# Optimization experiments

Hardware: AMD Instinct MI355X
Metric: run time of the kernel (lower is better)

The kernel has to match this reference:

```python
import jax, jax.numpy as jnp
import numpy as np

INPUT_SIZE = 4
HIDDEN_SIZE = 4
SEQ_LEN = 2048
BATCH = 4096


def _lstm_layer(x, W_ih, W_hh, b_ih, b_hh):
    """Single-layer LSTM over x: [T, B, I]; PyTorch gate order (i, f, g, o)."""
    H = W_hh.shape[1]
    B = x.shape[1]
    # Precompute the input projection for all timesteps (one big GEMM).
    xg = jnp.einsum('tbi,gi->tbg', x, W_ih) + (b_ih + b_hh)  # [T, B, 4H]

    def step(carry, xg_t):
        h, c = carry
        gates = xg_t + h @ W_hh.T  # [B, 4H]
        i, f, g, o = jnp.split(gates, 4, axis=-1)
        i = jax.nn.sigmoid(i)
        f = jax.nn.sigmoid(f)
        g = jnp.tanh(g)
        o = jax.nn.sigmoid(o)
        c = f * c + i * g
        h = o * jnp.tanh(c)
        return (h, c), h

    h0 = jnp.zeros((B, H), x.dtype)
    c0 = jnp.zeros((B, H), x.dtype)
    _, ys = jax.lax.scan(step, (h0, c0), xg)
    return ys  # [T, B, H]


def setup_inputs() -> dict:
    key = jax.random.key(0)
    ks = jax.random.split(key, 9)
    bound = 1.0 / np.sqrt(HIDDEN_SIZE)  # torch LSTM init: U(-1/sqrt(H), 1/sqrt(H))

    def u(k, shape):
        return jax.random.uniform(k, shape, jnp.float32, -bound, bound)

    x = jax.random.normal(ks[0], (SEQ_LEN, BATCH, INPUT_SIZE), jnp.float32)
    return {
        'x': x,
        'W_ih0': u(ks[1], (4 * HIDDEN_SIZE, INPUT_SIZE)),
        'W_hh0': u(ks[2], (4 * HIDDEN_SIZE, HIDDEN_SIZE)),
        'b_ih0': u(ks[3], (4 * HIDDEN_SIZE,)),
        'b_hh0': u(ks[4], (4 * HIDDEN_SIZE,)),
        'W_ih1': u(ks[5], (4 * HIDDEN_SIZE, HIDDEN_SIZE)),
        'W_hh1': u(ks[6], (4 * HIDDEN_SIZE, HIDDEN_SIZE)),
        'b_ih1': u(ks[7], (4 * HIDDEN_SIZE,)),
        'b_hh1': u(ks[8], (4 * HIDDEN_SIZE,)),
    }


def reference(x, W_ih0, W_hh0, b_ih0, b_hh0, W_ih1, W_hh1, b_ih1, b_hh1):
    h1 = _lstm_layer(x, W_ih0, W_hh0, b_ih0, b_hh0)
    h2 = _lstm_layer(h1, W_ih1, W_hh1, b_ih1, b_hh1)
    return h2  # [T, B, H], matching `x, _ = self.lstm(x); return x`
```

## Files before the change

kernel.cpp:

```cpp
#include <hip/hip_runtime.h>

#define SEQ_T   2048
#define BATCH_N 4096
#define LOG2E   1.4426950408889634f
#define K_SEG   16
#define NSEG    (SEQ_T / K_SEG)

#define DPPF(v, ctrl) __int_as_float(__builtin_amdgcn_mov_dpp(__float_as_int(v), (ctrl), 0xF, 0xF, true))
#define RHM 0x141
#define MIR 0x140

__global__ __launch_bounds__(128, 2) void lstm2_split(
    const float* __restrict__ x,
    const float* __restrict__ Wih0, const float* __restrict__ Whh0,
    const float* __restrict__ bih0, const float* __restrict__ bhh0,
    const float* __restrict__ Wih1, const float* __restrict__ Whh1,
    const float* __restrict__ bih1, const float* __restrict__ bhh1,
    float* __restrict__ out)
{
    __shared__ float ring[32][4][4];

    const int wv    = threadIdx.x >> 6;
    const int lane  = threadIdx.x & 63;
    const int cpos  = lane >> 4;
    const int g16   = lane & 15;
    const int u     = g16 >> 2;
    const int r     = g16 & 3;
    const int row   = r * 4 + u;
    const int chain = blockIdx.x * 4 + cpos;
    const bool isA  = (wv == 0);

    const float srow = (r == 2) ? (-2.0f * LOG2E) : (-LOG2E);
    float win[4], whh[4], bb;
    if (isA) {
#pragma unroll
        for (int d = 0; d < 4; ++d) {
            win[d] = Wih0[row * 4 + d]       * srow;
            whh[d] = Whh0[row * 4 + (u ^ d)] * srow;
        }
        bb = (bih0[row] + bhh0[row]) * srow;
    } else {
#pragma unroll
        for (int d = 0; d < 4; ++d) {
            win[d] = Wih1[row * 4 + d]       * srow;
            whh[d] = Whh1[row * 4 + (u ^ d)] * srow;
        }
        bb = (bih1[row] + bhh1[row]) * srow;
    }
    const float csc = -2.0f * LOG2E;
    const float ka = (r == 2) ? 2.0f * csc : 1.0f;
    const float kb = (r == 2) ? -csc       : 0.0f;

    const char* __restrict__ xb = (const char*)x;
    char* __restrict__ ob = (char*)out;

    float h = 0.f, ha = 0.f, hb2 = 0.f, hc = 0.f;
    float cs = 0.f;

    auto cell = [&](float acc) {
        acc = fmaf(whh[0], h, fmaf(whh[1], ha,
              fmaf(whh[2], hb2, fmaf(whh[3], hc, acc))));
        float e = __builtin_amdgcn_exp2f(acc);
        float s = __builtin_amdgcn_rcpf(1.0f + e);
        float a = fmaf(ka, s, kb);
        float iv = DPPF(a, 0x00), fv = DPPF(a, 0x55);
        float gv = DPPF(a, 0xAA), ov = DPPF(a, 0xFF);
        cs = fmaf(fv, cs, iv * gv);
        float z  = __builtin_amdgcn_exp2f(cs);
        float t2 = fmaf(2.0f, __builtin_amdgcn_rcpf(1.0f + z), -1.0f);
        h  = ov * t2;
        ha = DPPF(h, RHM);
        hc = DPPF(h, MIR);
        hb2 = DPPF(ha, MIR);
    };

    if (isA) {
        const unsigned xhome = (unsigned)chain * 16u;
        const unsigned XCL   = xhome + 2047u * 65536u;
        float4 xbuf[8];
        unsigned xoff = xhome;
#pragma unroll
        for (int i = 0; i < 8; ++i) {
            xbuf[i] = *(const float4*)(xb + xoff);
            xoff += 65536u;
        }
        for (int seg = 0; seg <= NSEG; ++seg) {
            __syncthreads();
            if (seg < NSEG) {
                float (*slot)[4] = ring[(seg & 1) * K_SEG];
#pragma unroll
                for (int i = 0; i < K_SEG; ++i) {
                    const float4 xv = xbuf[i & 7];
                    unsigned off = (xoff < XCL) ? xoff : XCL;
                    xbuf[i & 7] = *(const float4*)(xb + off);
                    xoff += 65536u;
                    float acc = fmaf(win[0], xv.x, fmaf(win[1], xv.y,
                                fmaf(win[2], xv.z, fmaf(win[3], xv.w, bb))));
                    cell(acc);
                    if (r == 0) slot[i * 4 + cpos][u] = h;
                }
            }
        }
    } else {
        unsigned ooff = (unsigned)(chain * 16 + u * 4);
        for (int seg = 0; seg <= NSEG; ++seg) {
            __syncthreads();
            if (seg > 0) {
                const float (*slot)[4] = ring[((seg - 1) & 1) * K_SEG];
                float4 hr[8];
#pragma unroll
                for (int hf = 0; hf < 2; ++hf) {
#pragma unroll
                    for (int s = 0; s < 8; ++s)
                        hr[s] = *(const float4*)&slot[(hf * 8 + s) * 4 + cpos][0];
#pragma unroll
                    for (int i = 0; i < 8; ++i) {
                        const float4 X = hr[i];
                        float acc = fmaf(win[0], X.x, fmaf(win[1], X.y,
                                    fmaf(win[2], X.z, fmaf(win[3], X.w, bb))));
                        cell(acc);
                        if (r == 0) *(float*)(ob + ooff) = h;
                        ooff += 65536u;
                    }
                }
            }
        }
    }
}

extern "C" void kernel_launch(void* const* d_in, const int* in_sizes, int n_in,
                              void* d_out, int out_size, void* d_ws, size_t ws_size,
                              hipStream_t stream) {
    const float* x    = (const float*)d_in[0];
    const float* Wih0 = (const float*)d_in[1];
    const float* Whh0 = (const float*)d_in[2];
    const float* bih0 = (const float*)d_in[3];
    const float* bhh0 = (const float*)d_in[4];
    const float* Wih1 = (const float*)d_in[5];
    const float* Whh1 = (const float*)d_in[6];
    const float* bih1 = (const float*)d_in[7];
    const float* bhh1 = (const float*)d_in[8];
    float* out = (float*)d_out;

    dim3 grid(1024), block(128);
    hipLaunchKernelGGL(lstm2_split, grid, block, 0, stream,
                       x, Wih0, Whh0, bih0, bhh0, Wih1, Whh1, bih1, bhh1, out);
}
```

Baseline: 258.8 us.

## Move layer-1 input projection into layer-0 wave and pass preactivations via LDS

The layer-0 wave now also computes the layer-1 input projection (W_ih1·h + bias) right after each step and writes one preactivation per gate row into a widened LDS ring. The layer-1 wave then only reads a scalar per step and runs the recurrent cell, which takes four FMAs off its serial critical path. The last segment is peeled so the x-load address clamp only runs there. In exchange the layer-0 wave does more work per step, every lane now writes to LDS, and the shared ring is four times larger.

```diff
diff --git a/kernel.cpp b/kernel.cpp
--- a/kernel.cpp
+++ b/kernel.cpp
@@ -18,7 +18,7 @@
     const float* __restrict__ bih1, const float* __restrict__ bhh1,
     float* __restrict__ out)
 {
-    __shared__ float ring[32][4][4];
+    __shared__ float ring[32][4][16];
 
     const int wv    = threadIdx.x >> 6;
     const int lane  = threadIdx.x & 63;
@@ -31,31 +31,12 @@
     const bool isA  = (wv == 0);
 
     const float srow = (r == 2) ? (-2.0f * LOG2E) : (-LOG2E);
-    float win[4], whh[4], bb;
-    if (isA) {
-#pragma unroll
-        for (int d = 0; d < 4; ++d) {
-            win[d] = Wih0[row * 4 + d]       * srow;
-            whh[d] = Whh0[row * 4 + (u ^ d)] * srow;
-        }
-        bb = (bih0[row] + bhh0[row]) * srow;
-    } else {
-#pragma unroll
-        for (int d = 0; d < 4; ++d) {
-            win[d] = Wih1[row * 4 + d]       * srow;
-            whh[d] = Whh1[row * 4 + (u ^ d)] * srow;
-        }
-        bb = (bih1[row] + bhh1[row]) * srow;
-    }
     const float csc = -2.0f * LOG2E;
     const float ka = (r == 2) ? 2.0f * csc : 1.0f;
     const float kb = (r == 2) ? -csc       : 0.0f;
 
-    const char* __restrict__ xb = (const char*)x;
-    char* __restrict__ ob = (char*)out;
-
-    float h = 0.f, ha = 0.f, hb2 = 0.f, hc = 0.f;
-    float cs = 0.f;
+    float whh[4];
+    float h = 0.f, ha = 0.f, hb2 = 0.f, hc = 0.f, cs = 0.f;
 
     auto cell = [&](float acc) {
         acc = fmaf(whh[0], h, fmaf(whh[1], ha,
@@ -74,7 +55,20 @@
         hb2 = DPPF(ha, MIR);
     };
 
+    const char* __restrict__ xb = (const char*)x;
+    char* __restrict__ ob = (char*)out;
+
     if (isA) {
+        float win[4], wpx[4];
+#pragma unroll
+        for (int d = 0; d < 4; ++d) {
+            win[d] = Wih0[row * 4 + d]       * srow;
+            whh[d] = Whh0[row * 4 + (u ^ d)] * srow;
+            wpx[d] = Wih1[row * 4 + (u ^ d)] * srow;
+        }
+        const float bb  = (bih0[row] + bhh0[row]) * srow;
+        const float bpx = (bih1[row] + bhh1[row]) * srow;
+
         const unsigned xhome = (unsigned)chain * 16u;
         const unsigned XCL   = xhome + 2047u * 65536u;
         float4 xbuf[8];
@@ -87,41 +81,56 @@
         for (int seg = 0; seg <= NSEG; ++seg) {
             __syncthreads();
             if (seg < NSEG) {
-                float (*slot)[4] = ring[(seg & 1) * K_SEG];
+                const int sb = (seg & 1) * K_SEG;
+                if (seg < NSEG - 1) {
 #pragma unroll
-                for (int i = 0; i < K_SEG; ++i) {
-                    const float4 xv = xbuf[i & 7];
-                    unsigned off = (xoff < XCL) ? xoff : XCL;
-                    xbuf[i & 7] = *(const float4*)(xb + off);
-                    xoff += 65536u;
-                    float acc = fmaf(win[0], xv.x, fmaf(win[1], xv.y,
-                                fmaf(win[2], xv.z, fmaf(win[3], xv.w, bb))));
-                    cell(acc);
-                    if (r == 0) slot[i * 4 + cpos][u] = h;
+                    for (int i = 0; i < K_SEG; ++i) {
+                        const float4 xv = xbuf[i & 7];
+                        xbuf[i & 7] = *(const float4*)(xb + xoff);
+                        xoff += 65536u;
+                        float acc = fmaf(win[0], xv.x, fmaf(win[1], xv.y,
+                                    fmaf(win[2], xv.z, fmaf(win[3], xv.w, bb))));
+                        cell(acc);
+                        float px = fmaf(wpx[0], h, fmaf(wpx[1], ha,
+                                   fmaf(wpx[2], hb2, fmaf(wpx[3], hc, bpx))));
+                        ring[sb + i][cpos][row] = px;
+                    }
+                } else {
+#pragma unroll
+                    for (int i = 0; i < K_SEG; ++i) {
+                        const float4 xv = xbuf[i & 7];
+                        unsigned off = (xoff < XCL) ? xoff : XCL;
+                        xbuf[i & 7] = *(const float4*)(xb + off);
+                        xoff += 65536u;
+                        float acc = fmaf(win[0], xv.x, fmaf(win[1], xv.y,
+                                    fmaf(win[2], xv.z, fmaf(win[3], xv.w, bb))));
+                        cell(acc);
+                        float px = fmaf(wpx[0], h, fmaf(wpx[1], ha,
+                                   fmaf(wpx[2], hb2, fmaf(wpx[3], hc, bpx))));
+                        ring[sb + i][cpos][row] = px;
+                    }
                 }
             }
         }
     } else {
+#pragma unroll
+        for (int d = 0; d < 4; ++d)
+            whh[d] = Whh1[row * 4 + (u ^ d)] * srow;
+
         unsigned ooff = (unsigned)(chain * 16 + u * 4);
         for (int seg = 0; seg <= NSEG; ++seg) {
             __syncthreads();
             if (seg > 0) {
-                const float (*slot)[4] = ring[((seg - 1) & 1) * K_SEG];
-                float4 hr[8];
+                const int sb = ((seg - 1) & 1) * K_SEG;
+                float pxr[K_SEG];
 #pragma unroll
-                for (int hf = 0; hf < 2; ++hf) {
+                for (int i = 0; i < K_SEG; ++i)
+                    pxr[i] = ring[sb + i][cpos][row];
 #pragma unroll
-                    for (int s = 0; s < 8; ++s)
-                        hr[s] = *(const float4*)&slot[(hf * 8 + s) * 4 + cpos][0];
-#pragma unroll
-                    for (int i = 0; i < 8; ++i) {
-                        const float4 X = hr[i];
-                        float acc = fmaf(win[0], X.x, fmaf(win[1], X.y,
-                                    fmaf(win[2], X.z, fmaf(win[3], X.w, bb))));
-                        cell(acc);
-                        if (r == 0) *(float*)(ob + ooff) = h;
-                        ooff += 65536u;
-                    }
+                for (int i = 0; i < K_SEG; ++i) {
+                    cell(pxr[i]);
+                    if (r == 0) *(float*)(ob + ooff) = h;
+                    ooff += 65536u;
                 }
             }
         }
```

Result: slower. 318.1 us (+22.9%).
